# Performance work log

Hardware: AMD Instinct MI355X
Metric: run time of the kernel (lower is better)

## Reference

```python
import jax, jax.numpy as jnp
import numpy as np

B, C, NC, H, W = 8, 128, 19, 128, 256
EPS = 1e-5


def ste_round(x):
    # straight-through-estimator round (Brevitas-style)
    return x + jax.lax.stop_gradient(jnp.round(x) - x)


def quant_weight(w):
    # int4 symmetric per-output-channel fake-quant: levels [-7, 7]
    s = jnp.maximum(jnp.max(jnp.abs(w), axis=(1, 2, 3), keepdims=True) / 7.0, 1e-8)
    wq = jnp.clip(ste_round(w / s), -7.0, 7.0) * s
    return wq, s


def quant_relu(x, s):
    # ReLU + uint4 fake-quant with learned per-tensor scale: levels [0, 15]
    return jnp.clip(ste_round(x / s), 0.0, 15.0) * s


def batchnorm(x, g, b, m, v):
    scale = (g / jnp.sqrt(v + EPS))[None, :, None, None]
    return (x - m[None, :, None, None]) * scale + b[None, :, None, None]


def dwconv3x3(x, w):
    # w: [C,1,3,3], groups=C
    return jax.lax.conv_general_dilated(
        x, w, window_strides=(1, 1), padding=((1, 1), (1, 1)),
        dimension_numbers=('NCHW', 'OIHW', 'NCHW'),
        feature_group_count=x.shape[1])


def pwconv(x, w):
    # 1x1 conv as einsum; w: [O,I,1,1]
    return jnp.einsum('bchw,oc->bohw', x, w[:, :, 0, 0])


def dsconv(x, dw_w, bn1, s1, pw_w, bn2, s2):
    wq, _ = quant_weight(dw_w)
    x = dwconv3x3(x, wq)
    x = batchnorm(x, *bn1)
    x = quant_relu(x, s1)
    wq, _ = quant_weight(pw_w)
    x = pwconv(x, wq)
    x = batchnorm(x, *bn2)
    x = quant_relu(x, s2)
    return x


def setup_inputs() -> dict:
    key = jax.random.key(0)
    ks = jax.random.split(key, 16)
    d = {}
    d['x'] = jax.random.normal(ks[0], (B, C, H, W), dtype=jnp.float32)
    d['dw1_w'] = jax.random.normal(ks[1], (C, 1, 3, 3), dtype=jnp.float32) * 0.1
    d['pw1_w'] = jax.random.normal(ks[2], (C, C, 1, 1), dtype=jnp.float32) * 0.05
    d['dw2_w'] = jax.random.normal(ks[3], (C, 1, 3, 3), dtype=jnp.float32) * 0.1
    d['pw2_w'] = jax.random.normal(ks[4], (C, C, 1, 1), dtype=jnp.float32) * 0.05
    d['cls_w'] = jax.random.normal(ks[5], (NC, C, 1, 1), dtype=jnp.float32) * 0.05
    d['cls_b'] = jax.random.normal(ks[6], (NC,), dtype=jnp.float32) * 0.1
    for i, kk in zip(range(1, 5), ks[7:11]):
        sub = jax.random.split(kk, 4)
        d[f'bn{i}_g'] = 1.0 + 0.1 * jax.random.normal(sub[0], (C,), dtype=jnp.float32)
        d[f'bn{i}_b'] = 0.1 * jax.random.normal(sub[1], (C,), dtype=jnp.float32)
        d[f'bn{i}_m'] = 0.1 * jax.random.normal(sub[2], (C,), dtype=jnp.float32)
        d[f'bn{i}_v'] = jax.random.uniform(sub[3], (C,), dtype=jnp.float32, minval=0.5, maxval=1.5)
    d['s_a1'] = jnp.float32(0.2)
    d['s_a2'] = jnp.float32(0.2)
    d['s_a3'] = jnp.float32(0.2)
    d['s_a4'] = jnp.float32(0.2)
    return d


def reference(x, dw1_w, pw1_w, dw2_w, pw2_w, cls_w, cls_b,
              bn1_g, bn1_b, bn1_m, bn1_v,
              bn2_g, bn2_b, bn2_m, bn2_v,
              bn3_g, bn3_b, bn3_m, bn3_v,
              bn4_g, bn4_b, bn4_m, bn4_v,
              s_a1, s_a2, s_a3, s_a4):
    x = dsconv(x, dw1_w, (bn1_g, bn1_b, bn1_m, bn1_v), s_a1,
               pw1_w, (bn2_g, bn2_b, bn2_m, bn2_v), s_a2)
    x = dsconv(x, dw2_w, (bn3_g, bn3_b, bn3_m, bn3_v), s_a3,
               pw2_w, (bn4_g, bn4_b, bn4_m, bn4_v), s_a4)
    # QuantDropout p=0.1 is identity in eval mode
    wq, sw = quant_weight(cls_w)
    # IntBias: bias quantized with scale = act_scale * weight_scale (per out channel)
    sb = s_a4 * sw[:, 0, 0, 0]
    bq = ste_round(cls_b / sb) * sb
    out = pwconv(x, wq) + bq[None, :, None, None]
    return out
```

## Files before the change

kernel.cpp:

```cpp
#include <hip/hip_runtime.h>

typedef __attribute__((ext_vector_type(4))) float f32x4;
typedef __attribute__((ext_vector_type(8))) short bf16x8;
typedef __attribute__((ext_vector_type(2))) unsigned int u32x2;
typedef __attribute__((ext_vector_type(4))) unsigned int u32x4;

#define EPSV 1e-5f

#define OFF_BUFA 0u
#define OFF_BUFB 33554432u
#define OFF_T    67108864u
#define OFF_WQ1  (OFF_T + 0u)
#define OFF_R3F  (OFF_T + 6144u)
#define OFF_CST3 (OFF_T + 10752u)
#define OFF_CST1 (OFF_T + 12800u)
#define OFF_R2BF (OFF_T + 14848u)
#define OFF_CST2 (OFF_T + 47616u)
#define OFF_R4BF (OFF_T + 49664u)
#define OFF_CST4 (OFF_T + 82432u)
#define OFF_R5BF (OFF_T + 84480u)
#define OFF_CST5 (OFF_T + 92672u)

struct PArgs {
  const float *dw1, *pw1, *dw2, *pw2, *clsw, *clsb;
  const float *g1, *b1, *m1, *v1;
  const float *g2, *b2, *m2, *v2;
  const float *g3, *b3, *m3, *v3;
  const float *g4, *b4, *m4, *v4;
  const float *s1, *s2, *s3, *s4;
};

__device__ __forceinline__ unsigned short f2bf(float f) {
  return (unsigned short)(__builtin_bit_cast(unsigned int, f) >> 16);
}
__device__ __forceinline__ float clip7(float r) { return fminf(fmaxf(r, -7.f), 7.f); }

__device__ __forceinline__ float bnval(float a, f32x4 c) {
  return (a * c.x - c.z) * c.y + c.w;
}

__device__ __forceinline__ void qstep4(float t0, float t1, float t2, float t3,
                                       float s, float rs,
                                       float &k0, float &k1, float &k2, float &k3) {
  float u0 = t0 * rs, u1 = t1 * rs, u2 = t2 * rs, u3 = t3 * rs;
  float f0 = rintf(u0), f1 = rintf(u1), f2 = rintf(u2), f3 = rintf(u3);
  float d0 = fabsf(fabsf(u0 - f0) - 0.5f);
  float d1 = fabsf(fabsf(u1 - f1) - 0.5f);
  float d2 = fabsf(fabsf(u2 - f2) - 0.5f);
  float d3 = fabsf(fabsf(u3 - f3) - 0.5f);
  bool near = (d0 < 3e-5f) | (d1 < 3e-5f) | (d2 < 3e-5f) | (d3 < 3e-5f);
  if (__any(near)) {
    f0 = rintf(t0 / s); f1 = rintf(t1 / s);
    f2 = rintf(t2 / s); f3 = rintf(t3 / s);
  }
  k0 = fminf(fmaxf(f0, 0.f), 15.f);
  k1 = fminf(fmaxf(f1, 0.f), 15.f);
  k2 = fminf(fmaxf(f2, 0.f), 15.f);
  k3 = fminf(fmaxf(f3, 0.f), 15.f);
}

__device__ __forceinline__ void cvt2(unsigned int d, unsigned int &lo, unsigned int &hi) {
  float f0 = (float)(d & 0xffu);
  float f1 = (float)((d >> 8) & 0xffu);
  float f2 = (float)((d >> 16) & 0xffu);
  float f3 = (float)(d >> 24);
  lo = (__builtin_bit_cast(unsigned int, f0) >> 16) | (__builtin_bit_cast(unsigned int, f1) & 0xffff0000u);
  hi = (__builtin_bit_cast(unsigned int, f2) >> 16) | (__builtin_bit_cast(unsigned int, f3) & 0xffff0000u);
}

__device__ __forceinline__ float wmax16(float v) {
  #pragma unroll
  for (int s = 1; s < 16; s <<= 1) v = fmaxf(v, __shfl_xor(v, s));
  return v;
}
__device__ __forceinline__ float wmax64(float v) {
  #pragma unroll
  for (int s = 1; s < 64; s <<= 1) v = fmaxf(v, __shfl_xor(v, s));
  return v;
}

__global__ __launch_bounds__(64) void prep_kernel(PArgs P, char* __restrict__ ws) {
  int bi = blockIdx.x, l = threadIdx.x;
  float* wq1 = (float*)(ws + OFF_WQ1);
  float* r3f = (float*)(ws + OFF_R3F);
  f32x4* cst1 = (f32x4*)(ws + OFF_CST1);
  f32x4* cst2 = (f32x4*)(ws + OFF_CST2);
  f32x4* cst3 = (f32x4*)(ws + OFF_CST3);
  f32x4* cst4 = (f32x4*)(ws + OFF_CST4);
  unsigned short* r2 = (unsigned short*)(ws + OFF_R2BF);
  unsigned short* r4 = (unsigned short*)(ws + OFF_R4BF);
  unsigned short* r5 = (unsigned short*)(ws + OFF_R5BF);
  float2* cst5 = (float2*)(ws + OFF_CST5);

  if (bi < 128) {
    int c = bi;
    float w = (l < 9) ? P.dw1[c * 9 + l] : 0.f;
    float mx = wmax16(fabsf(w));
    float sq = fmaxf(mx / 7.0f, 1e-8f);
    if (l < 9) wq1[c * 12 + l] = clip7(rintf(w / sq)) * sq;
    if (l == 0) {
      float sc = P.g1[c] / sqrtf(P.v1[c] + EPSV);
      cst1[c] = f32x4{1.f, sc, P.m1[c], P.b1[c]};
    }
  } else if (bi < 256) {
    int o = bi - 128;
    float w0 = P.pw1[o * 128 + l], w1 = P.pw1[o * 128 + 64 + l];
    float mx = wmax64(fmaxf(fabsf(w0), fabsf(w1)));
    float sq = fmaxf(mx / 7.0f, 1e-8f);
    r2[o * 128 + l]      = f2bf(clip7(rintf(w0 / sq)));
    r2[o * 128 + 64 + l] = f2bf(clip7(rintf(w1 / sq)));
    if (l == 0) {
      float sc = P.g2[o] / sqrtf(P.v2[o] + EPSV);
      cst2[o] = f32x4{P.s1[0] * sq, sc, P.m2[o], P.b2[o]};
    }
  } else if (bi < 384) {
    int c = bi - 256;
    float w = (l < 9) ? P.dw2[c * 9 + l] : 0.f;
    float mx = wmax16(fabsf(w));
    float sq = fmaxf(mx / 7.0f, 1e-8f);
    if (l < 9) r3f[l * 128 + c] = clip7(rintf(w / sq));
    if (l == 0) {
      float sc = P.g3[c] / sqrtf(P.v3[c] + EPSV);
      cst3[c] = f32x4{P.s2[0] * sq, sc, P.m3[c], P.b3[c]};
    }
  } else if (bi < 512) {
    int o = bi - 384;
    float w0 = P.pw2[o * 128 + l], w1 = P.pw2[o * 128 + 64 + l];
    float mx = wmax64(fmaxf(fabsf(w0), fabsf(w1)));
    float sq = fmaxf(mx / 7.0f, 1e-8f);
    r4[o * 128 + l]      = f2bf(clip7(rintf(w0 / sq)));
    r4[o * 128 + 64 + l] = f2bf(clip7(rintf(w1 / sq)));
    if (l == 0) {
      float sc = P.g4[o] / sqrtf(P.v4[o] + EPSV);
      cst4[o] = f32x4{P.s3[0] * sq, sc, P.m4[o], P.b4[o]};
    }
  } else {
    int o = bi - 512;
    if (o < 19) {
      float w0 = P.clsw[o * 128 + l], w1 = P.clsw[o * 128 + 64 + l];
      float mx = wmax64(fmaxf(fabsf(w0), fabsf(w1)));
      float sq = fmaxf(mx / 7.0f, 1e-8f);
      r5[o * 128 + l]      = f2bf(clip7(rintf(w0 / sq)));
      r5[o * 128 + 64 + l] = f2bf(clip7(rintf(w1 / sq)));
      if (l == 0) {
        float A5 = P.s4[0] * sq;
        float bq = rintf(P.clsb[o] / A5) * A5;
        cst5[o] = make_float2(A5, bq);
      }
    } else {
      r5[o * 128 + l] = 0; r5[o * 128 + 64 + l] = 0;
      if (l == 0) cst5[o] = make_float2(0.f, 0.f);
    }
  }
}

__global__ __launch_bounds__(512) void dwA_kernel(const float* __restrict__ x,
                                                  char* __restrict__ ws,
                                                  const float* __restrict__ s1p) {
  int bid = blockIdx.x;
  int b = bid & 7, c = bid >> 3;
  int tid = threadIdx.x;
  int wq = tid & 63, wv = tid >> 6;
  int w0 = wq << 2;
  int h0 = wv << 4;
  const float* wp = (const float*)(ws + OFF_WQ1) + c * 12;
  float k0 = wp[0], k1 = wp[1], k2 = wp[2], k3 = wp[3], k4 = wp[4],
        k5 = wp[5], k6 = wp[6], k7 = wp[7], k8 = wp[8];
  f32x4 cs = ((const f32x4*)(ws + OFF_CST1))[c];
  float s_act = *s1p;
  float rs = 1.0f / s_act;
  const float* plane = x + (((size_t)((b << 7) | c)) << 15);
  unsigned char* oplane = (unsigned char*)(ws + OFF_BUFB) + (((size_t)((b << 7) | c)) << 15);

  f32x4 vm = {0.f, 0.f, 0.f, 0.f};
  if (h0 > 0) vm = *(const f32x4*)(plane + ((h0 - 1) << 8) + w0);
  f32x4 v0 = *(const f32x4*)(plane + (h0 << 8) + w0);
  f32x4 vp = *(const f32x4*)(plane + ((h0 + 1) << 8) + w0);
  float lm = __shfl_up(vm.w, 1), l0 = __shfl_up(v0.w, 1), lp = __shfl_up(vp.w, 1);
  float rm = __shfl_down(vm.x, 1), r0 = __shfl_down(v0.x, 1), rp = __shfl_down(vp.x, 1);
  if (wq == 0)  { lm = 0.f; l0 = 0.f; lp = 0.f; }
  if (wq == 63) { rm = 0.f; r0 = 0.f; rp = 0.f; }

  #pragma unroll 4
  for (int i = 0; i < 16; i++) {
    int h = h0 + i;
    float y0 = 0.f, y1 = 0.f, y2 = 0.f, y3 = 0.f;
    y0 = fmaf(lm,   k0, y0); y0 = fmaf(vm.x, k1, y0); y0 = fmaf(vm.y, k2, y0);
    y1 = fmaf(vm.x, k0, y1); y1 = fmaf(vm.y, k1, y1); y1 = fmaf(vm.z, k2, y1);
    y2 = fmaf(vm.y, k0, y2); y2 = fmaf(vm.z, k1, y2); y2 = fmaf(vm.w, k2, y2);
    y3 = fmaf(vm.z, k0, y3); y3 = fmaf(vm.w, k1, y3); y3 = fmaf(rm,   k2, y3);

    y0 = fmaf(l0,   k3, y0); y0 = fmaf(v0.x, k4, y0); y0 = fmaf(v0.y, k5, y0);
    y1 = fmaf(v0.x, k3, y1); y1 = fmaf(v0.y, k4, y1); y1 = fmaf(v0.z, k5, y1);
    y2 = fmaf(v0.y, k3, y2); y2 = fmaf(v0.z, k4, y2); y2 = fmaf(v0.w, k5, y2);
    y3 = fmaf(v0.z, k3, y3); y3 = fmaf(v0.w, k4, y3); y3 = fmaf(r0,   k5, y3);

    y0 = fmaf(lp,   k6, y0); y0 = fmaf(vp.x, k7, y0); y0 = fmaf(vp.y, k8, y0);
    y1 = fmaf(vp.x, k6, y1); y1 = fmaf(vp.y, k7, y1); y1 = fmaf(vp.z, k8, y1);
    y2 = fmaf(vp.y, k6, y2); y2 = fmaf(vp.z, k7, y2); y2 = fmaf(vp.w, k8, y2);
    y3 = fmaf(vp.z, k6, y3); y3 = fmaf(vp.w, k7, y3); y3 = fmaf(rp,   k8, y3);

    float q0, q1, q2, q3;
    qstep4(bnval(y0, cs), bnval(y1, cs), bnval(y2, cs), bnval(y3, cs),
           s_act, rs, q0, q1, q2, q3);
    unsigned int pk = (unsigned int)q0 | ((unsigned int)q1 << 8) |
                      ((unsigned int)q2 << 16) | ((unsigned int)q3 << 24);
    *(unsigned int*)(oplane + (h << 8) + w0) = pk;

    vm = v0; lm = l0; rm = r0;
    v0 = vp; l0 = lp; r0 = rp;
    f32x4 nv = {0.f, 0.f, 0.f, 0.f};
    if (i < 15 && h + 2 < 128) nv = *(const f32x4*)(plane + ((h + 2) << 8) + w0);
    vp = nv;
    float nl = __shfl_up(nv.w, 1), nr = __shfl_down(nv.x, 1);
    if (wq == 0)  nl = 0.f;
    if (wq == 63) nr = 0.f;
    lp = nl; rp = nr;
  }
}

__global__ __launch_bounds__(256) void pwn_kernel(const unsigned char* __restrict__ in,
                                                  unsigned char* __restrict__ out,
                                                  const unsigned short* __restrict__ rbf,
                                                  const f32x4* __restrict__ cst,
                                                  const float* __restrict__ sp) {
  __shared__ unsigned char lds[32768];
  int tid = threadIdx.x;
  int p0 = blockIdx.x << 7;
  int b_img = p0 >> 15, loc0 = p0 & 32767;
  {
    int pb = tid & 7, cq = tid >> 3;
    int c4 = cq << 2;
    int kc = cq >> 3, lgr = (cq >> 1) & 3, half = cq & 1;
    const unsigned char* ib = in + (((size_t)(b_img << 7)) << 15) + loc0 + (pb << 4);
    u32x4 t0 = *(const u32x4*)(ib + ((size_t)(c4 + 0) << 15));
    u32x4 t1 = *(const u32x4*)(ib + ((size_t)(c4 + 1) << 15));
    u32x4 t2 = *(const u32x4*)(ib + ((size_t)(c4 + 2) << 15));
    u32x4 t3 = *(const u32x4*)(ib + ((size_t)(c4 + 3) << 15));
    int swz = (pb & 7) << 4;
    #pragma unroll
    for (int s = 0; s < 16; s++) {
      int wrd = s >> 2, sh8 = (s & 3) << 3;
      unsigned int chw = ((t0[wrd] >> sh8) & 0xffu)
                       | (((t1[wrd] >> sh8) & 0xffu) << 8)
                       | (((t2[wrd] >> sh8) & 0xffu) << 16)
                       | (((t3[wrd] >> sh8) & 0xffu) << 24);
      unsigned int lo, hi;
      cvt2(chw, lo, hi);
      int ad = ((((((pb << 2) + kc) << 6) | s | (lgr << 4)) << 4) + (half << 3)) ^ swz;
      *(u32x2*)(lds + ad) = u32x2{lo, hi};
    }
  }
  __syncthreads();
  int l = tid & 63, wv = tid >> 6;
  int ob = wv << 5;
  bf16x8 af[2][4];
  #pragma unroll
  for (int ot = 0; ot < 2; ot++)
    #pragma unroll
    for (int kc = 0; kc < 4; kc++) {
      int o = ob + (ot << 4) + (l & 15);
      int k = (kc << 5) + ((l >> 4) << 3);
      af[ot][kc] = *(const bf16x8*)(rbf + o * 128 + k);
    }
  f32x4 acc[2][8];
  #pragma unroll
  for (int ot = 0; ot < 2; ot++)
    #pragma unroll
    for (int pt = 0; pt < 8; pt++) acc[ot][pt] = f32x4{0.f, 0.f, 0.f, 0.f};
  #pragma unroll
  for (int kc = 0; kc < 4; kc++) {
    bf16x8 bb[8];
    #pragma unroll
    for (int pt = 0; pt < 8; pt++)
      bb[pt] = *(const bf16x8*)(lds + (((((((pt << 2) + kc) << 6)) + l) << 4) ^ ((pt & 7) << 4)));
    #pragma unroll
    for (int ot = 0; ot < 2; ot++)
      #pragma unroll
      for (int pt = 0; pt < 8; pt++)
        acc[ot][pt] = __builtin_amdgcn_mfma_f32_16x16x32_bf16(af[ot][kc], bb[pt], acc[ot][pt], 0, 0, 0);
  }
  float s_act = *sp;
  float rs = 1.0f / s_act;
  #pragma unroll
  for (int ot = 0; ot < 2; ot++) {
    int o0 = ob + (ot << 4) + ((l >> 4) << 2);
    f32x4 c0 = cst[o0], c1 = cst[o0 + 1], c2 = cst[o0 + 2], c3 = cst[o0 + 3];
    #pragma unroll
    for (int pt = 0; pt < 8; pt++) {
      int p = p0 + (pt << 4) + (l & 15);
      f32x4 a = acc[ot][pt];
      float q0, q1, q2, q3;
      qstep4(bnval(a.x, c0), bnval(a.y, c1), bnval(a.z, c2), bnval(a.w, c3),
             s_act, rs, q0, q1, q2, q3);
      unsigned int pk = (unsigned int)q0 | ((unsigned int)q1 << 8) |
                        ((unsigned int)q2 << 16) | ((unsigned int)q3 << 24);
      *(unsigned int*)(out + (size_t)p * 128 + o0) = pk;
    }
  }
}

__global__ __launch_bounds__(256) void dw2pwcls_kernel(const unsigned char* __restrict__ in,
                                                       float* __restrict__ out,
                                                       const char* __restrict__ ws,
                                                       const unsigned short* __restrict__ rbf,
                                                       const f32x4* __restrict__ cst,
                                                       const float* __restrict__ s3p,
                                                       const float* __restrict__ s4p,
                                                       const unsigned short* __restrict__ r5,
                                                       const float2* __restrict__ cst5) {
  __shared__ unsigned char lds[32768];
  int tid = threadIdx.x;
  int p0 = blockIdx.x << 7;
  {
    int cq = tid & 31, pg = tid >> 5;
    int c4 = cq << 2;
    const float* r3f = (const float*)(ws + OFF_R3F);
    float wk[9][4];
    #pragma unroll
    for (int t = 0; t < 9; t++) {
      wk[t][0] = r3f[t * 128 + c4];     wk[t][1] = r3f[t * 128 + c4 + 1];
      wk[t][2] = r3f[t * 128 + c4 + 2]; wk[t][3] = r3f[t * 128 + c4 + 3];
    }
    const f32x4* cst3 = (const f32x4*)(ws + OFF_CST3);
    f32x4 cs0 = cst3[c4], cs1 = cst3[c4 + 1], cs2 = cst3[c4 + 2], cs3 = cst3[c4 + 3];
    float s_act3 = *s3p;
    float rs3 = 1.0f / s_act3;
    int kc = c4 >> 5, hi = (c4 >> 3) & 3, half = (c4 >> 2) & 1;
    int g = hi | ((kc & 1) << 2);
    int hh = (p0 >> 8) & 127;
    #pragma unroll 2
    for (int ps = 0; ps < 4; ps++) {
      int pbase = p0 + (ps << 5) + (pg << 2);
      int wbase = pbase & 255;
      unsigned int xw[3][6];
      #pragma unroll
      for (int r = 0; r < 3; r++) {
        int gh = hh + r - 1;
        if (gh >= 0 && gh <= 127) {
          const unsigned char* rp = in + (size_t)(pbase + (r - 1) * 256) * 128 + c4;
          xw[r][0] = (wbase > 0)   ? *(const unsigned int*)(rp - 128) : 0u;
          xw[r][1] = *(const unsigned int*)(rp);
          xw[r][2] = *(const unsigned int*)(rp + 128);
          xw[r][3] = *(const unsigned int*)(rp + 256);
          xw[r][4] = *(const unsigned int*)(rp + 384);
          xw[r][5] = (wbase < 252) ? *(const unsigned int*)(rp + 512) : 0u;
        } else {
          xw[r][0] = 0u; xw[r][1] = 0u; xw[r][2] = 0u;
          xw[r][3] = 0u; xw[r][4] = 0u; xw[r][5] = 0u;
        }
      }
      #pragma unroll
      for (int j = 0; j < 4; j++) {
        float a0 = 0.f, a1 = 0.f, a2 = 0.f, a3 = 0.f;
        #pragma unroll
        for (int r = 0; r < 3; r++) {
          #pragma unroll
          for (int dwi = 0; dwi < 3; dwi++) {
            unsigned int v = xw[r][j + dwi];
            int t = r * 3 + dwi;
            a0 = fmaf((float)(v & 0xffu),         wk[t][0], a0);
            a1 = fmaf((float)((v >> 8) & 0xffu),  wk[t][1], a1);
            a2 = fmaf((float)((v >> 16) & 0xffu), wk[t][2], a2);
            a3 = fmaf((float)(v >> 24),           wk[t][3], a3);
          }
        }
        float k0f, k1f, k2f, k3f;
        qstep4(bnval(a0, cs0), bnval(a1, cs1), bnval(a2, cs2), bnval(a3, cs3),
               s_act3, rs3, k0f, k1f, k2f, k3f);
        unsigned int wlo = (__builtin_bit_cast(unsigned int, k0f) >> 16) |
                           (__builtin_bit_cast(unsigned int, k1f) & 0xffff0000u);
        unsigned int whi = (__builtin_bit_cast(unsigned int, k2f) >> 16) |
                           (__builtin_bit_cast(unsigned int, k3f) & 0xffff0000u);
        int p_local = (ps << 5) + (pg << 2) + j;
        int pt = p_local >> 4, pl = p_local & 15;
        int slot = (pl ^ g) | (hi << 4);
        int ad = (((((pt << 2) + kc) << 6) | slot) << 4) + (half << 3);
        *(u32x2*)(lds + ad) = u32x2{wlo, whi};
      }
    }
  }
  __syncthreads();
  int l = tid & 63, wv = tid >> 6;
  int ob = wv << 5;
  bf16x8 af[2][4];
  #pragma unroll
  for (int ot = 0; ot < 2; ot++)
    #pragma unroll
    for (int kc = 0; kc < 4; kc++) {
      int o = ob + (ot << 4) + (l & 15);
      int k = (kc << 5) + ((l >> 4) << 3);
      af[ot][kc] = *(const bf16x8*)(rbf + o * 128 + k);
    }
  f32x4 acc[2][8];
  #pragma unroll
  for (int ot = 0; ot < 2; ot++)
    #pragma unroll
    for (int pt = 0; pt < 8; pt++) acc[ot][pt] = f32x4{0.f, 0.f, 0.f, 0.f};
  #pragma unroll
  for (int kc = 0; kc < 4; kc++) {
    int gg = (l >> 4) | ((kc & 1) << 2);
    bf16x8 bb[8];
    #pragma unroll
    for (int pt = 0; pt < 8; pt++)
      bb[pt] = *(const bf16x8*)(lds + ((((((pt << 2) + kc) << 6)) | (l ^ gg)) << 4));
    #pragma unroll
    for (int ot = 0; ot < 2; ot++)
      #pragma unroll
      for (int pt = 0; pt < 8; pt++)
        acc[ot][pt] = __builtin_amdgcn_mfma_f32_16x16x32_bf16(af[ot][kc], bb[pt], acc[ot][pt], 0, 0, 0);
  }
  float s_act4 = *s4p;
  float rs4 = 1.0f / s_act4;
  __syncthreads();
  {
    int hsel = (l >> 4) & 1;
    #pragma unroll
    for (int ot = 0; ot < 2; ot++) {
      int o0 = ob + (ot << 4) + ((l >> 4) << 2);
      f32x4 c0 = cst[o0], c1 = cst[o0 + 1], c2 = cst[o0 + 2], c3 = cst[o0 + 3];
      int hi = (ot << 1) + ((l >> 4) >> 1);
      int lfrag = (l & 15) | (hi << 4);
      #pragma unroll
      for (int pt = 0; pt < 8; pt++) {
        f32x4 a = acc[ot][pt];
        float k0f, k1f, k2f, k3f;
        qstep4(bnval(a.x, c0), bnval(a.y, c1), bnval(a.z, c2), bnval(a.w, c3),
               s_act4, rs4, k0f, k1f, k2f, k3f);
        unsigned int w0 = (__builtin_bit_cast(unsigned int, k0f) >> 16) |
                          (__builtin_bit_cast(unsigned int, k1f) & 0xffff0000u);
        unsigned int w1 = (__builtin_bit_cast(unsigned int, k2f) >> 16) |
                          (__builtin_bit_cast(unsigned int, k3f) & 0xffff0000u);
        int ad = (((((pt << 2) + wv) << 6) | lfrag) << 4) + (hsel << 3);
        *(u32x2*)(lds + ad) = u32x2{w0, w1};
      }
    }
  }
  __syncthreads();
  int pt0 = wv << 1;
  bf16x8 af5[2][4];
  #pragma unroll
  for (int ot = 0; ot < 2; ot++)
    #pragma unroll
    for (int kc = 0; kc < 4; kc++) {
      int o = (ot << 4) + (l & 15);
      int k = (kc << 5) + ((l >> 4) << 3);
      af5[ot][kc] = *(const bf16x8*)(r5 + o * 128 + k);
    }
  f32x4 a5[2][2] = {{{0,0,0,0},{0,0,0,0}},{{0,0,0,0},{0,0,0,0}}};
  #pragma unroll
  for (int kc = 0; kc < 4; kc++) {
    bf16x8 b0 = *(const bf16x8*)(lds + ((((((pt0    ) << 2) + kc) << 6) + l) << 4));
    bf16x8 b1 = *(const bf16x8*)(lds + ((((((pt0 + 1) << 2) + kc) << 6) + l) << 4));
    #pragma unroll
    for (int ot = 0; ot < 2; ot++) {
      a5[ot][0] = __builtin_amdgcn_mfma_f32_16x16x32_bf16(af5[ot][kc], b0, a5[ot][0], 0, 0, 0);
      a5[ot][1] = __builtin_amdgcn_mfma_f32_16x16x32_bf16(af5[ot][kc], b1, a5[ot][1], 0, 0, 0);
    }
  }
  #pragma unroll
  for (int ptl = 0; ptl < 2; ptl++) {
    int p = p0 + ((pt0 + ptl) << 4) + (l & 15);
    int bb = p >> 15, hw = p & 32767;
    float* ob2 = out + (((size_t)bb * 19) << 15) + hw;
    #pragma unroll
    for (int ot = 0; ot < 2; ot++) {
      int obase = (ot << 4) + ((l >> 4) << 2);
      f32x4 a = a5[ot][ptl];
      #pragma unroll
      for (int i = 0; i < 4; i++) {
        int o = obase + i;
        if (o < 19) {
          float2 c5 = cst5[o];
          ob2[(size_t)o << 15] = fmaf(a[i], c5.x, c5.y);
        }
      }
    }
  }
}

extern "C" void kernel_launch(void* const* d_in, const int* in_sizes, int n_in,
                              void* d_out, int out_size, void* d_ws, size_t ws_size,
                              hipStream_t stream) {
  (void)in_sizes; (void)n_in; (void)out_size; (void)ws_size;
  char* ws = (char*)d_ws;
  PArgs P;
  P.dw1  = (const float*)d_in[1];
  P.pw1  = (const float*)d_in[2];
  P.dw2  = (const float*)d_in[3];
  P.pw2  = (const float*)d_in[4];
  P.clsw = (const float*)d_in[5];
  P.clsb = (const float*)d_in[6];
  P.g1 = (const float*)d_in[7];  P.b1 = (const float*)d_in[8];
  P.m1 = (const float*)d_in[9];  P.v1 = (const float*)d_in[10];
  P.g2 = (const float*)d_in[11]; P.b2 = (const float*)d_in[12];
  P.m2 = (const float*)d_in[13]; P.v2 = (const float*)d_in[14];
  P.g3 = (const float*)d_in[15]; P.b3 = (const float*)d_in[16];
  P.m3 = (const float*)d_in[17]; P.v3 = (const float*)d_in[18];
  P.g4 = (const float*)d_in[19]; P.b4 = (const float*)d_in[20];
  P.m4 = (const float*)d_in[21]; P.v4 = (const float*)d_in[22];
  P.s1 = (const float*)d_in[23]; P.s2 = (const float*)d_in[24];
  P.s3 = (const float*)d_in[25]; P.s4 = (const float*)d_in[26];

  const float* x = (const float*)d_in[0];
  unsigned char* bufA = (unsigned char*)(ws + OFF_BUFA);
  unsigned char* bufB = (unsigned char*)(ws + OFF_BUFB);

  prep_kernel<<<544, 64, 0, stream>>>(P, ws);
  dwA_kernel<<<1024, 512, 0, stream>>>(x, ws, P.s1);
  pwn_kernel<<<2048, 256, 0, stream>>>(bufB, bufA,
      (const unsigned short*)(ws + OFF_R2BF), (const f32x4*)(ws + OFF_CST2), P.s2);
  dw2pwcls_kernel<<<2048, 256, 0, stream>>>(bufA, (float*)d_out, ws,
      (const unsigned short*)(ws + OFF_R4BF), (const f32x4*)(ws + OFF_CST4),
      P.s3, P.s4,
      (const unsigned short*)(ws + OFF_R5BF), (const float2*)(ws + OFF_CST5));
}
```

Baseline: 128.0 us.

## Split fused dw2+pw+cls kernel into separate dw2 and pw+cls kernels

Un-fuses the second depthwise conv from the pointwise/classifier kernel: a new dw2_kernel writes the uint8 activation to a global buffer, and pwcls_kernel reloads it with vectorized loads into LDS. Both kernels and pwn_kernel also remap block indices so consecutive blocks land on different XCD-interleaved regions. The dw2 kernel stages its weight/BN tables in shared memory. This adds an extra 32MB write+read round trip but gives each kernel simpler structure and possibly better occupancy.

```diff
diff --git a/kernel.cpp b/kernel.cpp
--- a/kernel.cpp
+++ b/kernel.cpp
@@ -226,12 +226,14 @@
                                                   const float* __restrict__ sp) {
   __shared__ unsigned char lds[32768];
   int tid = threadIdx.x;
-  int p0 = blockIdx.x << 7;
+  int bid = blockIdx.x;
+  int sbid = ((bid & 7) << 8) | (bid >> 3);
+  int p0 = sbid << 7;
   int b_img = p0 >> 15, loc0 = p0 & 32767;
   {
     int pb = tid & 7, cq = tid >> 3;
     int c4 = cq << 2;
-    int kc = cq >> 3, lgr = (cq >> 1) & 3, half = cq & 1;
+    int kc = cq >> 3, lgr = (cq >> 1) & 3, hlf = cq & 1;
     const unsigned char* ib = in + (((size_t)(b_img << 7)) << 15) + loc0 + (pb << 4);
     u32x4 t0 = *(const u32x4*)(ib + ((size_t)(c4 + 0) << 15));
     u32x4 t1 = *(const u32x4*)(ib + ((size_t)(c4 + 1) << 15));
@@ -247,7 +249,7 @@
                        | (((t3[wrd] >> sh8) & 0xffu) << 24);
       unsigned int lo, hi;
       cvt2(chw, lo, hi);
-      int ad = ((((((pb << 2) + kc) << 6) | s | (lgr << 4)) << 4) + (half << 3)) ^ swz;
+      int ad = ((((((pb << 2) + kc) << 6) | s | (lgr << 4)) << 4) + (hlf << 3)) ^ swz;
       *(u32x2*)(lds + ad) = u32x2{lo, hi};
     }
   }
@@ -300,85 +302,97 @@
   }
 }
 
-__global__ __launch_bounds__(256) void dw2pwcls_kernel(const unsigned char* __restrict__ in,
-                                                       float* __restrict__ out,
-                                                       const char* __restrict__ ws,
-                                                       const unsigned short* __restrict__ rbf,
-                                                       const f32x4* __restrict__ cst,
-                                                       const float* __restrict__ s3p,
-                                                       const float* __restrict__ s4p,
-                                                       const unsigned short* __restrict__ r5,
-                                                       const float2* __restrict__ cst5) {
+__global__ __launch_bounds__(256) void dw2_kernel(const unsigned char* __restrict__ in,
+                                                  unsigned char* __restrict__ out,
+                                                  const char* __restrict__ ws,
+                                                  const float* __restrict__ sp) {
+  __shared__ float tabs[1664];
+  const float* src = (const float*)(ws + OFF_R3F);
+  for (int i = threadIdx.x; i < 1664; i += 256) tabs[i] = src[i];
+  __syncthreads();
+  int tid = threadIdx.x;
+  int cq = tid & 31, pg = tid >> 5;
+  int c4 = cq << 2;
+  float wk[9][4];
+  #pragma unroll
+  for (int t = 0; t < 9; t++) {
+    wk[t][0] = tabs[t * 128 + c4];     wk[t][1] = tabs[t * 128 + c4 + 1];
+    wk[t][2] = tabs[t * 128 + c4 + 2]; wk[t][3] = tabs[t * 128 + c4 + 3];
+  }
+  const f32x4* cst3 = (const f32x4*)(tabs + 1152);
+  f32x4 cs0 = cst3[c4], cs1 = cst3[c4 + 1], cs2 = cst3[c4 + 2], cs3 = cst3[c4 + 3];
+  float s_act = *sp;
+  float rs = 1.0f / s_act;
+  int bid = blockIdx.x;
+  int sbid = ((bid & 7) << 10) | (bid >> 3);
+  int pbase = (sbid << 5) + (pg << 2);
+  int wbase = pbase & 255, hh = (pbase >> 8) & 127;
+
+  unsigned int xw[3][6];
+  #pragma unroll
+  for (int r = 0; r < 3; r++) {
+    int gh = hh + r - 1;
+    if (gh >= 0 && gh <= 127) {
+      const unsigned char* rp = in + (size_t)(pbase + (r - 1) * 256) * 128 + c4;
+      xw[r][0] = (wbase > 0)   ? *(const unsigned int*)(rp - 128) : 0u;
+      xw[r][1] = *(const unsigned int*)(rp);
+      xw[r][2] = *(const unsigned int*)(rp + 128);
+      xw[r][3] = *(const unsigned int*)(rp + 256);
+      xw[r][4] = *(const unsigned int*)(rp + 384);
+      xw[r][5] = (wbase < 252) ? *(const unsigned int*)(rp + 512) : 0u;
+    } else {
+      xw[r][0] = 0u; xw[r][1] = 0u; xw[r][2] = 0u;
+      xw[r][3] = 0u; xw[r][4] = 0u; xw[r][5] = 0u;
+    }
+  }
+  #pragma unroll
+  for (int j = 0; j < 4; j++) {
+    float a0 = 0.f, a1 = 0.f, a2 = 0.f, a3 = 0.f;
+    #pragma unroll
+    for (int r = 0; r < 3; r++) {
+      #pragma unroll
+      for (int dwi = 0; dwi < 3; dwi++) {
+        unsigned int v = xw[r][j + dwi];
+        int t = r * 3 + dwi;
+        a0 = fmaf((float)(v & 0xffu),         wk[t][0], a0);
+        a1 = fmaf((float)((v >> 8) & 0xffu),  wk[t][1], a1);
+        a2 = fmaf((float)((v >> 16) & 0xffu), wk[t][2], a2);
+        a3 = fmaf((float)(v >> 24),           wk[t][3], a3);
+      }
+    }
+    float q0, q1, q2, q3;
+    qstep4(bnval(a0, cs0), bnval(a1, cs1), bnval(a2, cs2), bnval(a3, cs3),
+           s_act, rs, q0, q1, q2, q3);
+    unsigned int pk = (unsigned int)q0 | ((unsigned int)q1 << 8) |
+                      ((unsigned int)q2 << 16) | ((unsigned int)q3 << 24);
+    *(unsigned int*)(out + (size_t)(pbase + j) * 128 + c4) = pk;
+  }
+}
+
+__global__ __launch_bounds__(256) void pwcls_kernel(const unsigned char* __restrict__ in,
+                                                    float* __restrict__ out,
+                                                    const unsigned short* __restrict__ rbf,
+                                                    const f32x4* __restrict__ cst,
+                                                    const float* __restrict__ sp,
+                                                    const unsigned short* __restrict__ r5,
+                                                    const float2* __restrict__ cst5) {
   __shared__ unsigned char lds[32768];
   int tid = threadIdx.x;
-  int p0 = blockIdx.x << 7;
-  {
-    int cq = tid & 31, pg = tid >> 5;
-    int c4 = cq << 2;
-    const float* r3f = (const float*)(ws + OFF_R3F);
-    float wk[9][4];
-    #pragma unroll
-    for (int t = 0; t < 9; t++) {
-      wk[t][0] = r3f[t * 128 + c4];     wk[t][1] = r3f[t * 128 + c4 + 1];
-      wk[t][2] = r3f[t * 128 + c4 + 2]; wk[t][3] = r3f[t * 128 + c4 + 3];
-    }
-    const f32x4* cst3 = (const f32x4*)(ws + OFF_CST3);
-    f32x4 cs0 = cst3[c4], cs1 = cst3[c4 + 1], cs2 = cst3[c4 + 2], cs3 = cst3[c4 + 3];
-    float s_act3 = *s3p;
-    float rs3 = 1.0f / s_act3;
-    int kc = c4 >> 5, hi = (c4 >> 3) & 3, half = (c4 >> 2) & 1;
-    int g = hi | ((kc & 1) << 2);
-    int hh = (p0 >> 8) & 127;
-    #pragma unroll 2
-    for (int ps = 0; ps < 4; ps++) {
-      int pbase = p0 + (ps << 5) + (pg << 2);
-      int wbase = pbase & 255;
-      unsigned int xw[3][6];
-      #pragma unroll
-      for (int r = 0; r < 3; r++) {
-        int gh = hh + r - 1;
-        if (gh >= 0 && gh <= 127) {
-          const unsigned char* rp = in + (size_t)(pbase + (r - 1) * 256) * 128 + c4;
-          xw[r][0] = (wbase > 0)   ? *(const unsigned int*)(rp - 128) : 0u;
-          xw[r][1] = *(const unsigned int*)(rp);
-          xw[r][2] = *(const unsigned int*)(rp + 128);
-          xw[r][3] = *(const unsigned int*)(rp + 256);
-          xw[r][4] = *(const unsigned int*)(rp + 384);
-          xw[r][5] = (wbase < 252) ? *(const unsigned int*)(rp + 512) : 0u;
-        } else {
-          xw[r][0] = 0u; xw[r][1] = 0u; xw[r][2] = 0u;
-          xw[r][3] = 0u; xw[r][4] = 0u; xw[r][5] = 0u;
-        }
-      }
-      #pragma unroll
-      for (int j = 0; j < 4; j++) {
-        float a0 = 0.f, a1 = 0.f, a2 = 0.f, a3 = 0.f;
-        #pragma unroll
-        for (int r = 0; r < 3; r++) {
-          #pragma unroll
-          for (int dwi = 0; dwi < 3; dwi++) {
-            unsigned int v = xw[r][j + dwi];
-            int t = r * 3 + dwi;
-            a0 = fmaf((float)(v & 0xffu),         wk[t][0], a0);
-            a1 = fmaf((float)((v >> 8) & 0xffu),  wk[t][1], a1);
-            a2 = fmaf((float)((v >> 16) & 0xffu), wk[t][2], a2);
-            a3 = fmaf((float)(v >> 24),           wk[t][3], a3);
-          }
-        }
-        float k0f, k1f, k2f, k3f;
-        qstep4(bnval(a0, cs0), bnval(a1, cs1), bnval(a2, cs2), bnval(a3, cs3),
-               s_act3, rs3, k0f, k1f, k2f, k3f);
-        unsigned int wlo = (__builtin_bit_cast(unsigned int, k0f) >> 16) |
-                           (__builtin_bit_cast(unsigned int, k1f) & 0xffff0000u);
-        unsigned int whi = (__builtin_bit_cast(unsigned int, k2f) >> 16) |
-                           (__builtin_bit_cast(unsigned int, k3f) & 0xffff0000u);
-        int p_local = (ps << 5) + (pg << 2) + j;
-        int pt = p_local >> 4, pl = p_local & 15;
-        int slot = (pl ^ g) | (hi << 4);
-        int ad = (((((pt << 2) + kc) << 6) | slot) << 4) + (half << 3);
-        *(u32x2*)(lds + ad) = u32x2{wlo, whi};
-      }
-    }
+  int bid = blockIdx.x;
+  int sbid = ((bid & 7) << 8) | (bid >> 3);
+  int p0 = sbid << 7;
+  #pragma unroll
+  for (int it = 0; it < 4; it++) {
+    int idx = tid + (it << 8);
+    int p = idx >> 3, q = idx & 7;
+    int kc = q >> 1, lg = (q & 1) << 1, pt = p >> 4;
+    u32x4 g = *(const u32x4*)(in + (size_t)(p0 + p) * 128 + q * 16);
+    unsigned int a0, a1, a2, a3, a4, a5, a6, a7;
+    cvt2(g.x, a0, a1); cvt2(g.y, a2, a3); cvt2(g.z, a4, a5); cvt2(g.w, a6, a7);
+    int l1 = (p & 15) | (lg << 4);
+    int ad = (((((pt << 2) + kc) << 6) | l1) << 4);
+    *(u32x4*)(lds + ad)       = u32x4{a0, a1, a2, a3};
+    *(u32x4*)(lds + ad + 256) = u32x4{a4, a5, a6, a7};
   }
   __syncthreads();
   int l = tid & 63, wv = tid >> 6;
@@ -399,19 +413,18 @@
     for (int pt = 0; pt < 8; pt++) acc[ot][pt] = f32x4{0.f, 0.f, 0.f, 0.f};
   #pragma unroll
   for (int kc = 0; kc < 4; kc++) {
-    int gg = (l >> 4) | ((kc & 1) << 2);
     bf16x8 bb[8];
     #pragma unroll
     for (int pt = 0; pt < 8; pt++)
-      bb[pt] = *(const bf16x8*)(lds + ((((((pt << 2) + kc) << 6)) | (l ^ gg)) << 4));
+      bb[pt] = *(const bf16x8*)(lds + ((((((pt << 2) + kc) << 6)) + l) << 4));
     #pragma unroll
     for (int ot = 0; ot < 2; ot++)
       #pragma unroll
       for (int pt = 0; pt < 8; pt++)
         acc[ot][pt] = __builtin_amdgcn_mfma_f32_16x16x32_bf16(af[ot][kc], bb[pt], acc[ot][pt], 0, 0, 0);
   }
-  float s_act4 = *s4p;
-  float rs4 = 1.0f / s_act4;
+  float s_act = *sp;
+  float rs = 1.0f / s_act;
   __syncthreads();
   {
     int hsel = (l >> 4) & 1;
@@ -426,7 +439,7 @@
         f32x4 a = acc[ot][pt];
         float k0f, k1f, k2f, k3f;
         qstep4(bnval(a.x, c0), bnval(a.y, c1), bnval(a.z, c2), bnval(a.w, c3),
-               s_act4, rs4, k0f, k1f, k2f, k3f);
+               s_act, rs, k0f, k1f, k2f, k3f);
         unsigned int w0 = (__builtin_bit_cast(unsigned int, k0f) >> 16) |
                           (__builtin_bit_cast(unsigned int, k1f) & 0xffff0000u);
         unsigned int w1 = (__builtin_bit_cast(unsigned int, k2f) >> 16) |
@@ -510,8 +523,8 @@
   dwA_kernel<<<1024, 512, 0, stream>>>(x, ws, P.s1);
   pwn_kernel<<<2048, 256, 0, stream>>>(bufB, bufA,
       (const unsigned short*)(ws + OFF_R2BF), (const f32x4*)(ws + OFF_CST2), P.s2);
-  dw2pwcls_kernel<<<2048, 256, 0, stream>>>(bufA, (float*)d_out, ws,
-      (const unsigned short*)(ws + OFF_R4BF), (const f32x4*)(ws + OFF_CST4),
-      P.s3, P.s4,
+  dw2_kernel<<<8192, 256, 0, stream>>>(bufA, bufB, ws, P.s3);
+  pwcls_kernel<<<2048, 256, 0, stream>>>(bufB, (float*)d_out,
+      (const unsigned short*)(ws + OFF_R4BF), (const f32x4*)(ws + OFF_CST4), P.s4,
       (const unsigned short*)(ws + OFF_R5BF), (const float2*)(ws + OFF_CST5));
 }
```

New measurement: 136.3 us. 1.07x slower.
